# Performance work log

Hardware: AMD Instinct MI355X
Metric: run time of the kernel (lower is better)

The kernel has to match this reference:

```python
import jax, jax.numpy as jnp
import numpy as np

EPS = 1e-5
HEADS = 8
DIM_KEY = 128
K = 16           # num_experts_per_head
NUM_KEYS = 256   # sqrt(num_experts)


def setup_inputs() -> dict:
    key = jax.random.key(0)
    ks = jax.random.split(key, 5)
    B, T, D = 1, 1024, 1024
    x = jax.random.normal(ks[0], (B, T, D), dtype=jnp.float32)
    norm_w = jnp.ones((D,), dtype=jnp.float32)
    wq = jax.random.normal(ks[1], (D, DIM_KEY * HEADS * 2), dtype=jnp.float32) * 0.02
    keys = jax.random.normal(ks[2], (HEADS, NUM_KEYS, 2, DIM_KEY), dtype=jnp.float32) * 0.02
    expert_down = jax.random.normal(ks[3], (NUM_KEYS * NUM_KEYS, D), dtype=jnp.float32) * 0.02
    expert_up = jax.random.normal(ks[4], (NUM_KEYS * NUM_KEYS, D), dtype=jnp.float32) * 0.02
    return {"x": x, "norm_w": norm_w, "wq": wq, "keys": keys,
            "expert_down": expert_down, "expert_up": expert_up}


def reference(x, norm_w, wq, keys, expert_down, expert_up):
    B, T, D = x.shape
    # RMSNorm
    inv = jax.lax.rsqrt(jnp.mean(x * x, axis=-1, keepdims=True) + EPS)
    x_norm = x * inv * norm_w                                   # [B,T,D]
    # queries -> [B,T,H,2,dk]
    q = (x_norm @ wq).reshape(B, T, HEADS, 2, DIM_KEY)
    # similarity with product keys: sim[p] for each of the two sub-key sets
    sim = jnp.einsum('bthpd,hkpd->pbthk', q, keys)              # [2,B,T,H,NUM_KEYS]
    s1, i1 = jax.lax.top_k(sim[0], K)                           # [B,T,H,K]
    s2, i2 = jax.lax.top_k(sim[1], K)
    # cartesian product of the two top-k sets
    all_idx = (i1[..., :, None] * NUM_KEYS + i2[..., None, :]).reshape(B, T, HEADS, K * K)
    all_scores = (s1[..., :, None] + s2[..., None, :]).reshape(B, T, HEADS, K * K)
    final_scores, pk = jax.lax.top_k(all_scores, K)             # [B,T,H,K]
    final_idx = jnp.take_along_axis(all_idx, pk, axis=-1)       # [B,T,H,K]
    # gather expert vectors
    wd = expert_down[final_idx]                                 # [B,T,H,K,D]
    wu = expert_up[final_idx]                                   # [B,T,H,K,D]
    hidden = jnp.einsum('btd,bthkd->bthk', x_norm, wd)
    hidden = jax.nn.gelu(hidden, approximate=False)             # torch nn.GELU default = erf
    hidden = hidden * jax.nn.relu(final_scores)
    out = jnp.einsum('bthk,bthkd->btd', hidden, wu)             # [B,T,D]
    return out
```

## Files before the change

### kernel.cpp

```cpp
#include <hip/hip_runtime.h>
#include <hip/hip_bf16.h>
#include <math.h>

#define T_TOK   1024
#define D_MODEL 1024
#define H_HEADS 8
#define DKEY    128
#define NKEYS   256
#define TOPK    16
#define TPB     4

__device__ __forceinline__ float dot4(float4 a, float4 b){
  return a.x*b.x + a.y*b.y + a.z*b.z + a.w*b.w;
}

__global__ __launch_bounds__(256) void k_rmsnorm(const float* __restrict__ x,
                                                 const float* __restrict__ nw,
                                                 float* __restrict__ xn)
{
  const int t = blockIdx.x, tid = threadIdx.x;
  const float4 v = *(const float4*)(x + (size_t)t*D_MODEL + tid*4);
  float ss = dot4(v, v);
  #pragma unroll
  for (int m = 1; m < 64; m <<= 1) ss += __shfl_xor(ss, m, 64);
  __shared__ float part[4];
  const int lane = tid & 63, wid = tid >> 6;
  if (lane == 0) part[wid] = ss;
  __syncthreads();
  const float tot = part[0] + part[1] + part[2] + part[3];
  const float inv = rsqrtf(tot * (1.0f/(float)D_MODEL) + 1e-5f);
  const float4 w = *(const float4*)(nw + tid*4);
  float4 o;
  o.x = v.x*inv*w.x; o.y = v.y*inv*w.y; o.z = v.z*inv*w.z; o.w = v.w*inv*w.w;
  *(float4*)(xn + (size_t)t*D_MODEL + tid*4) = o;
}

#define TBM 64
#define TBN 64
#define TBK 16
__global__ __launch_bounds__(256) void k_qgemm(const float* __restrict__ A,
                                               const float* __restrict__ B,
                                               float* __restrict__ C)
{
  const int N = 2048, Kd = 1024;
  __shared__ float As[TBK][TBM+4];
  __shared__ float Bs[TBK][TBN+4];
  const int tid = threadIdx.x;
  const int row0 = blockIdx.y * TBM, col0 = blockIdx.x * TBN;
  const int ar = tid >> 2,  ac = (tid & 3) * 4;
  const int br = tid >> 4,  bc = (tid & 15) * 4;
  const int ty = tid >> 4,  tx = tid & 15;
  float acc[4][4] = {{0}};
  for (int k0 = 0; k0 < Kd; k0 += TBK){
    const float4 a = *(const float4*)(A + (size_t)(row0+ar)*Kd + k0 + ac);
    const float4 b = *(const float4*)(B + (size_t)(k0+br)*N + col0 + bc);
    As[ac+0][ar] = a.x; As[ac+1][ar] = a.y; As[ac+2][ar] = a.z; As[ac+3][ar] = a.w;
    *(float4*)&Bs[br][bc] = b;
    __syncthreads();
    #pragma unroll
    for (int kk = 0; kk < TBK; kk++){
      const float4 av = *(const float4*)&As[kk][ty*4];
      const float4 bv = *(const float4*)&Bs[kk][tx*4];
      acc[0][0] += av.x*bv.x; acc[0][1] += av.x*bv.y; acc[0][2] += av.x*bv.z; acc[0][3] += av.x*bv.w;
      acc[1][0] += av.y*bv.x; acc[1][1] += av.y*bv.y; acc[1][2] += av.y*bv.z; acc[1][3] += av.y*bv.w;
      acc[2][0] += av.z*bv.x; acc[2][1] += av.z*bv.y; acc[2][2] += av.z*bv.z; acc[2][3] += av.z*bv.w;
      acc[3][0] += av.w*bv.x; acc[3][1] += av.w*bv.y; acc[3][2] += av.w*bv.z; acc[3][3] += av.w*bv.w;
    }
    __syncthreads();
  }
  #pragma unroll
  for (int i = 0; i < 4; i++){
    float4 o; o.x = acc[i][0]; o.y = acc[i][1]; o.z = acc[i][2]; o.w = acc[i][3];
    *(float4*)(C + (size_t)(row0 + ty*4 + i)*N + col0 + tx*4) = o;
  }
}

__global__ __launch_bounds__(256) void k_simgemm(const float* __restrict__ Q,
                                                 const float* __restrict__ keys,
                                                 float* __restrict__ sims)
{
  const int hp = blockIdx.z;
  const int t0 = blockIdx.y * 64, kb0 = blockIdx.x * 64;
  const float* A = Q + (size_t)t0*2048 + (hp>>1)*256 + (hp&1)*128;
  const float* B = keys + ((size_t)((hp>>1)*NKEYS + kb0)*2 + (hp&1)) * DKEY;
  __shared__ float As[TBK][64+4];
  __shared__ float Bs[TBK][64+4];
  const int tid = threadIdx.x;
  const int ar = tid >> 2, ac = (tid & 3) * 4;
  const int ty = tid >> 4, tx = tid & 15;
  float acc[4][4] = {{0}};
  for (int kd = 0; kd < DKEY; kd += TBK){
    const float4 a = *(const float4*)(A + (size_t)ar*2048 + kd + ac);
    const float4 b = *(const float4*)(B + (size_t)ar*256  + kd + ac);
    As[ac+0][ar] = a.x; As[ac+1][ar] = a.y; As[ac+2][ar] = a.z; As[ac+3][ar] = a.w;
    Bs[ac+0][ar] = b.x; Bs[ac+1][ar] = b.y; Bs[ac+2][ar] = b.z; Bs[ac+3][ar] = b.w;
    __syncthreads();
    #pragma unroll
    for (int kk = 0; kk < TBK; kk++){
      const float4 av = *(const float4*)&As[kk][ty*4];
      const float4 bv = *(const float4*)&Bs[kk][tx*4];
      acc[0][0] += av.x*bv.x; acc[0][1] += av.x*bv.y; acc[0][2] += av.x*bv.z; acc[0][3] += av.x*bv.w;
      acc[1][0] += av.y*bv.x; acc[1][1] += av.y*bv.y; acc[1][2] += av.y*bv.z; acc[1][3] += av.y*bv.w;
      acc[2][0] += av.z*bv.x; acc[2][1] += av.z*bv.y; acc[2][2] += av.z*bv.z; acc[2][3] += av.z*bv.w;
      acc[3][0] += av.w*bv.x; acc[3][1] += av.w*bv.y; acc[3][2] += av.w*bv.z; acc[3][3] += av.w*bv.w;
    }
    __syncthreads();
  }
  float* Cb = sims + (size_t)t0*4096 + hp*256 + kb0;
  #pragma unroll
  for (int i = 0; i < 4; i++){
    float4 o; o.x = acc[i][0]; o.y = acc[i][1]; o.z = acc[i][2]; o.w = acc[i][3];
    *(float4*)(Cb + (size_t)(ty*4 + i)*4096 + tx*4) = o;
  }
}

__device__ __forceinline__ void wave_top16(float v[4], int lane, float* tvO, int* tiO)
{
  for (int r = 0; r < 16; r++){
    float bv = v[0]; int bj = 0;
    #pragma unroll
    for (int j = 1; j < 4; j++) if (v[j] > bv){ bv = v[j]; bj = j; }
    int bi = lane*4 + bj;
    #pragma unroll
    for (int m = 1; m < 64; m <<= 1){
      const float ov = __shfl_xor(bv, m, 64);
      const int   oi = __shfl_xor(bi, m, 64);
      if (ov > bv || (ov == bv && oi < bi)){ bv = ov; bi = oi; }
    }
    if (lane == 0){ tvO[r] = bv; tiO[r] = bi; }
    if ((bi >> 2) == lane) v[bi & 3] = -INFINITY;
  }
}

__global__ __launch_bounds__(256) void k_topk(const float* __restrict__ sims,
                                              int* __restrict__ fidxO,
                                              float* __restrict__ gateO)
{
  const int h  = blockIdx.x;
  const int t0 = blockIdx.y * TPB;
  const int tid = threadIdx.x;
  const int w = tid >> 6, lane = tid & 63;
  const int t = t0 + w;
  __shared__ float tv[TPB][2][TOPK];
  __shared__ int   ti[TPB][2][TOPK];

  float v0[4], v1[4];
  {
    const float4 a = *(const float4*)(sims + (size_t)t*4096 + (h*2+0)*256 + lane*4);
    const float4 b = *(const float4*)(sims + (size_t)t*4096 + (h*2+1)*256 + lane*4);
    v0[0]=a.x; v0[1]=a.y; v0[2]=a.z; v0[3]=a.w;
    v1[0]=b.x; v1[1]=b.y; v1[2]=b.z; v1[3]=b.w;
  }
  wave_top16(v0, lane, &tv[w][0][0], &ti[w][0][0]);
  wave_top16(v1, lane, &tv[w][1][0], &ti[w][1][0]);

  float cv[4];
  const int i0 = lane >> 2;
  #pragma unroll
  for (int j = 0; j < 4; j++)
    cv[j] = tv[w][0][i0] + tv[w][1][4*(lane & 3) + j];

  const size_t obase = (size_t)((t)*H_HEADS + h) * TOPK;
  for (int r = 0; r < 16; r++){
    float bv = cv[0]; int bj = 0;
    #pragma unroll
    for (int j = 1; j < 4; j++) if (cv[j] > bv){ bv = cv[j]; bj = j; }
    int bc = lane*4 + bj;
    #pragma unroll
    for (int m = 1; m < 64; m <<= 1){
      const float ov = __shfl_xor(bv, m, 64);
      const int   oc = __shfl_xor(bc, m, 64);
      if (ov > bv || (ov == bv && oc < bc)){ bv = ov; bc = oc; }
    }
    if (lane == 0){
      fidxO[obase + r] = ti[w][0][bc >> 4] * NKEYS + ti[w][1][bc & 15];
      gateO[obase + r] = bv > 0.0f ? bv : 0.0f;
    }
    if ((bc >> 2) == lane) cv[bc & 3] = -INFINITY;
  }
}

__global__ __launch_bounds__(256) void k_peer_down(const float* __restrict__ xn,
                                                   const float* __restrict__ ed,
                                                   const int* __restrict__ fidx,
                                                   const float* __restrict__ gate,
                                                   float* __restrict__ coeff)
{
  const int b = blockIdx.x;
  const int t = b >> 3;
  const int tid = threadIdx.x, w = tid >> 6, lane = tid & 63;
  const int base = b * TOPK;

  float4 xv[4];
  #pragma unroll
  for (int j = 0; j < 4; j++)
    xv[j] = *(const float4*)(xn + (size_t)t*D_MODEL + j*256 + lane*4);

  int e[4];
  #pragma unroll
  for (int r = 0; r < 4; r++) e[r] = fidx[base + w*4 + r];

  float4 wv[4][4];
  #pragma unroll
  for (int r = 0; r < 4; r++)
    #pragma unroll
    for (int j = 0; j < 4; j++)
      wv[r][j] = *(const float4*)(ed + (size_t)e[r]*D_MODEL + j*256 + lane*4);

  float s[4];
  #pragma unroll
  for (int r = 0; r < 4; r++){
    float p = dot4(wv[r][0], xv[0]) + dot4(wv[r][1], xv[1])
            + dot4(wv[r][2], xv[2]) + dot4(wv[r][3], xv[3]);
    #pragma unroll
    for (int m = 1; m < 64; m <<= 1) p += __shfl_xor(p, m, 64);
    s[r] = p;
  }
  if (lane < 4){
    const float hs = (lane == 0) ? s[0] : (lane == 1) ? s[1] : (lane == 2) ? s[2] : s[3];
    const float g = 0.5f * hs * (1.0f + erff(hs * 0.70710678118654752440f));
    coeff[base + w*4 + lane] = g * gate[base + w*4 + lane];
  }
}

__global__ __launch_bounds__(256) void k_peer_up(const float* __restrict__ eu,
                                                 const int* __restrict__ fidx,
                                                 const float* __restrict__ coeff,
                                                 float* __restrict__ out)
{
  const int t = blockIdx.x, tid = threadIdx.x;
  __shared__ int   sidx[H_HEADS*TOPK];
  __shared__ float sc[H_HEADS*TOPK];
  if (tid < H_HEADS*TOPK){
    sidx[tid] = fidx[(size_t)t*H_HEADS*TOPK + tid];
    sc[tid]   = coeff[(size_t)t*H_HEADS*TOPK + tid];
  }
  __syncthreads();
  float4 acc = {0.f, 0.f, 0.f, 0.f};
  for (int j = 0; j < H_HEADS*TOPK; j += 8){
    float4 wv[8];
    #pragma unroll
    for (int u = 0; u < 8; u++)
      wv[u] = *(const float4*)(eu + (size_t)sidx[j+u]*D_MODEL + tid*4);
    #pragma unroll
    for (int u = 0; u < 8; u++){
      const float c = sc[j+u];
      acc.x += c*wv[u].x; acc.y += c*wv[u].y; acc.z += c*wv[u].z; acc.w += c*wv[u].w;
    }
  }
  *(float4*)(out + (size_t)t*D_MODEL + tid*4) = acc;
}

extern "C" void kernel_launch(void* const* d_in, const int* in_sizes, int n_in,
                              void* d_out, int out_size, void* d_ws, size_t ws_size,
                              hipStream_t stream)
{
  const float* x      = (const float*)d_in[0];
  const float* norm_w = (const float*)d_in[1];
  const float* wq     = (const float*)d_in[2];
  const float* keys   = (const float*)d_in[3];
  const float* ed     = (const float*)d_in[4];
  const float* eu     = (const float*)d_in[5];
  float* out = (float*)d_out;

  float* xn   = (float*)d_ws;
  float* q    = xn + (size_t)T_TOK * D_MODEL;
  int*   fidx = (int*)(q + (size_t)T_TOK * 2048);
  float* gate = (float*)(fidx + (size_t)T_TOK * H_HEADS * TOPK);
  float* sims = gate + (size_t)T_TOK * H_HEADS * TOPK;
  float* coeff = sims;

  k_rmsnorm<<<T_TOK, 256, 0, stream>>>(x, norm_w, xn);
  k_qgemm<<<dim3(2048/TBN, 1024/TBM), 256, 0, stream>>>(xn, wq, q);
  k_simgemm<<<dim3(NKEYS/64, T_TOK/64, 16), 256, 0, stream>>>(q, keys, sims);
  k_topk<<<dim3(H_HEADS, T_TOK/TPB), 256, 0, stream>>>(sims, fidx, gate);
  k_peer_down<<<T_TOK*H_HEADS, 256, 0, stream>>>(xn, ed, fidx, gate, coeff);
  k_peer_up<<<T_TOK, 256, 0, stream>>>(eu, fidx, coeff, out);
}
```

Baseline: 323.3 us.

## Enlarge q-GEMM tiles with register prefetch double buffering; deepen sim-GEMM K tile

The query GEMM now uses 128x64 tiles with a 32-deep K slice and 8x4 outputs per thread. It double-buffers shared memory, prefetching the next slice into registers while computing the current one. This raises arithmetic intensity and hides global load latency, at the cost of more registers and LDS and fewer blocks (256). The similarity GEMM doubles its K tile to 32, halving its barrier count.

```diff
diff --git a/kernel.cpp b/kernel.cpp
--- a/kernel.cpp
+++ b/kernel.cpp
@@ -35,46 +35,79 @@
   *(float4*)(xn + (size_t)t*D_MODEL + tid*4) = o;
 }
 
-#define TBM 64
-#define TBN 64
-#define TBK 16
+#define QM 128
+#define QN 64
+#define QK 32
 __global__ __launch_bounds__(256) void k_qgemm(const float* __restrict__ A,
                                                const float* __restrict__ B,
                                                float* __restrict__ C)
 {
   const int N = 2048, Kd = 1024;
-  __shared__ float As[TBK][TBM+4];
-  __shared__ float Bs[TBK][TBN+4];
+  __shared__ float As[2][QK][QM+4];
+  __shared__ float Bs[2][QK][QN+4];
   const int tid = threadIdx.x;
-  const int row0 = blockIdx.y * TBM, col0 = blockIdx.x * TBN;
-  const int ar = tid >> 2,  ac = (tid & 3) * 4;
-  const int br = tid >> 4,  bc = (tid & 15) * 4;
-  const int ty = tid >> 4,  tx = tid & 15;
-  float acc[4][4] = {{0}};
-  for (int k0 = 0; k0 < Kd; k0 += TBK){
-    const float4 a = *(const float4*)(A + (size_t)(row0+ar)*Kd + k0 + ac);
-    const float4 b = *(const float4*)(B + (size_t)(k0+br)*N + col0 + bc);
-    As[ac+0][ar] = a.x; As[ac+1][ar] = a.y; As[ac+2][ar] = a.z; As[ac+3][ar] = a.w;
-    *(float4*)&Bs[br][bc] = b;
-    __syncthreads();
-    #pragma unroll
-    for (int kk = 0; kk < TBK; kk++){
-      const float4 av = *(const float4*)&As[kk][ty*4];
-      const float4 bv = *(const float4*)&Bs[kk][tx*4];
-      acc[0][0] += av.x*bv.x; acc[0][1] += av.x*bv.y; acc[0][2] += av.x*bv.z; acc[0][3] += av.x*bv.w;
-      acc[1][0] += av.y*bv.x; acc[1][1] += av.y*bv.y; acc[1][2] += av.y*bv.z; acc[1][3] += av.y*bv.w;
-      acc[2][0] += av.z*bv.x; acc[2][1] += av.z*bv.y; acc[2][2] += av.z*bv.z; acc[2][3] += av.z*bv.w;
-      acc[3][0] += av.w*bv.x; acc[3][1] += av.w*bv.y; acc[3][2] += av.w*bv.z; acc[3][3] += av.w*bv.w;
-    }
-    __syncthreads();
-  }
-  #pragma unroll
-  for (int i = 0; i < 4; i++){
+  const int row0 = blockIdx.y * QM, col0 = blockIdx.x * QN;
+  const int lr = tid >> 1,  lk  = (tid & 1) * 16;
+  const int br = tid >> 4,  bc  = (tid & 15) * 4;
+  const int ty = tid >> 4,  tx  = tid & 15;
+  float4 a0,a1,a2,a3,b0,b1;
+  float acc[8][4] = {{0}};
+
+  const float* Ap = A + (size_t)(row0+lr)*Kd + lk;
+  const float* Bp = B + (size_t)br*N + col0 + bc;
+
+  a0 = *(const float4*)(Ap+0);  a1 = *(const float4*)(Ap+4);
+  a2 = *(const float4*)(Ap+8);  a3 = *(const float4*)(Ap+12);
+  b0 = *(const float4*)(Bp);
+  b1 = *(const float4*)(Bp + (size_t)16*N);
+
+  #define QWRITE(P) do { \
+    As[P][lk+ 0][lr]=a0.x; As[P][lk+ 1][lr]=a0.y; As[P][lk+ 2][lr]=a0.z; As[P][lk+ 3][lr]=a0.w; \
+    As[P][lk+ 4][lr]=a1.x; As[P][lk+ 5][lr]=a1.y; As[P][lk+ 6][lr]=a1.z; As[P][lk+ 7][lr]=a1.w; \
+    As[P][lk+ 8][lr]=a2.x; As[P][lk+ 9][lr]=a2.y; As[P][lk+10][lr]=a2.z; As[P][lk+11][lr]=a2.w; \
+    As[P][lk+12][lr]=a3.x; As[P][lk+13][lr]=a3.y; As[P][lk+14][lr]=a3.z; As[P][lk+15][lr]=a3.w; \
+    *(float4*)&Bs[P][br][bc]    = b0; \
+    *(float4*)&Bs[P][br+16][bc] = b1; } while(0)
+
+  QWRITE(0);
+  __syncthreads();
+
+  for (int t = 0; t < Kd/QK; t++){
+    const int p = t & 1;
+    if (t < Kd/QK - 1){
+      const int k0n = (t+1)*QK;
+      a0 = *(const float4*)(Ap + k0n);      a1 = *(const float4*)(Ap + k0n + 4);
+      a2 = *(const float4*)(Ap + k0n + 8);  a3 = *(const float4*)(Ap + k0n + 12);
+      b0 = *(const float4*)(Bp + (size_t)k0n*N);
+      b1 = *(const float4*)(Bp + (size_t)(k0n+16)*N);
+    }
+    #pragma unroll
+    for (int kk = 0; kk < QK; kk++){
+      const float4 av0 = *(const float4*)&As[p][kk][ty*8];
+      const float4 av1 = *(const float4*)&As[p][kk][ty*8+4];
+      const float4 bv  = *(const float4*)&Bs[p][kk][tx*4];
+      const float af[8] = {av0.x,av0.y,av0.z,av0.w,av1.x,av1.y,av1.z,av1.w};
+      const float bf[4] = {bv.x,bv.y,bv.z,bv.w};
+      #pragma unroll
+      for (int i = 0; i < 8; i++)
+        #pragma unroll
+        for (int j = 0; j < 4; j++)
+          acc[i][j] += af[i] * bf[j];
+    }
+    if (t < Kd/QK - 1){
+      QWRITE(1-p);
+      __syncthreads();
+    }
+  }
+  #pragma unroll
+  for (int i = 0; i < 8; i++){
     float4 o; o.x = acc[i][0]; o.y = acc[i][1]; o.z = acc[i][2]; o.w = acc[i][3];
-    *(float4*)(C + (size_t)(row0 + ty*4 + i)*N + col0 + tx*4) = o;
-  }
-}
-
+    *(float4*)(C + (size_t)(row0 + ty*8 + i)*N + col0 + tx*4) = o;
+  }
+  #undef QWRITE
+}
+
+#define SBK 32
 __global__ __launch_bounds__(256) void k_simgemm(const float* __restrict__ Q,
                                                  const float* __restrict__ keys,
                                                  float* __restrict__ sims)
@@ -83,20 +116,24 @@
   const int t0 = blockIdx.y * 64, kb0 = blockIdx.x * 64;
   const float* A = Q + (size_t)t0*2048 + (hp>>1)*256 + (hp&1)*128;
   const float* B = keys + ((size_t)((hp>>1)*NKEYS + kb0)*2 + (hp&1)) * DKEY;
-  __shared__ float As[TBK][64+4];
-  __shared__ float Bs[TBK][64+4];
+  __shared__ float As[SBK][64+4];
+  __shared__ float Bs[SBK][64+4];
   const int tid = threadIdx.x;
   const int ar = tid >> 2, ac = (tid & 3) * 4;
   const int ty = tid >> 4, tx = tid & 15;
   float acc[4][4] = {{0}};
-  for (int kd = 0; kd < DKEY; kd += TBK){
-    const float4 a = *(const float4*)(A + (size_t)ar*2048 + kd + ac);
-    const float4 b = *(const float4*)(B + (size_t)ar*256  + kd + ac);
-    As[ac+0][ar] = a.x; As[ac+1][ar] = a.y; As[ac+2][ar] = a.z; As[ac+3][ar] = a.w;
-    Bs[ac+0][ar] = b.x; Bs[ac+1][ar] = b.y; Bs[ac+2][ar] = b.z; Bs[ac+3][ar] = b.w;
+  for (int kd = 0; kd < DKEY; kd += SBK){
+    const float4 a0 = *(const float4*)(A + (size_t)ar*2048 + kd + ac);
+    const float4 a1 = *(const float4*)(A + (size_t)ar*2048 + kd + ac + 16);
+    const float4 c0 = *(const float4*)(B + (size_t)ar*256  + kd + ac);
+    const float4 c1 = *(const float4*)(B + (size_t)ar*256  + kd + ac + 16);
+    As[ac+0][ar]=a0.x; As[ac+1][ar]=a0.y; As[ac+2][ar]=a0.z; As[ac+3][ar]=a0.w;
+    As[ac+16][ar]=a1.x; As[ac+17][ar]=a1.y; As[ac+18][ar]=a1.z; As[ac+19][ar]=a1.w;
+    Bs[ac+0][ar]=c0.x; Bs[ac+1][ar]=c0.y; Bs[ac+2][ar]=c0.z; Bs[ac+3][ar]=c0.w;
+    Bs[ac+16][ar]=c1.x; Bs[ac+17][ar]=c1.y; Bs[ac+18][ar]=c1.z; Bs[ac+19][ar]=c1.w;
     __syncthreads();
     #pragma unroll
-    for (int kk = 0; kk < TBK; kk++){
+    for (int kk = 0; kk < SBK; kk++){
       const float4 av = *(const float4*)&As[kk][ty*4];
       const float4 bv = *(const float4*)&Bs[kk][tx*4];
       acc[0][0] += av.x*bv.x; acc[0][1] += av.x*bv.y; acc[0][2] += av.x*bv.z; acc[0][3] += av.x*bv.w;
@@ -271,7 +308,7 @@
   float* coeff = sims;
 
   k_rmsnorm<<<T_TOK, 256, 0, stream>>>(x, norm_w, xn);
-  k_qgemm<<<dim3(2048/TBN, 1024/TBM), 256, 0, stream>>>(xn, wq, q);
+  k_qgemm<<<dim3(2048/QN, 1024/QM), 256, 0, stream>>>(xn, wq, q);
   k_simgemm<<<dim3(NKEYS/64, T_TOK/64, 16), 256, 0, stream>>>(q, keys, sims);
   k_topk<<<dim3(H_HEADS, T_TOK/TPB), 256, 0, stream>>>(sims, fidx, gate);
   k_peer_down<<<T_TOK*H_HEADS, 256, 0, stream>>>(xn, ed, fidx, gate, coeff);
```

Measured after the change: 336.8 us. +4.2%, slower.
